# Performance work log

Hardware: AMD Instinct MI355X
Metric: run time of the kernel (lower is better)

## Reference

```python
import jax, jax.numpy as jnp
import numpy as np

L, B, E = 8192, 2, 1024
H, WS = 16, 256
D = E // H


def setup_inputs() -> dict:
    key = jax.random.key(0)
    ks = jax.random.split(key, 8)
    mk = lambda k: jax.random.normal(k, (E, E), dtype=jnp.float32) * 0.02
    return {
        'query': jax.random.normal(ks[0], (L, B, E), dtype=jnp.float32),
        'key':   jax.random.normal(ks[1], (L, B, E), dtype=jnp.float32),
        'value': jax.random.normal(ks[2], (L, B, E), dtype=jnp.float32),
        'Wq': mk(ks[3]), 'bq': jnp.zeros((E,), jnp.float32),
        'Wk': mk(ks[4]), 'bk': jnp.zeros((E,), jnp.float32),
        'Wv': mk(ks[5]), 'bv': jnp.zeros((E,), jnp.float32),
        'Wo': mk(ks[6]), 'bo': jnp.zeros((E,), jnp.float32),
    }


def reference(query, key, value, Wq, bq, Wk, bk, Wv, bv, Wo, bo):
    # Faithful translation, including the original's (B,L,H,D) layout and the
    # raw-memory view(B,H,L//ws,ws,D) reinterpretation of that layout.
    proj = lambda x, W, b: x @ W.T + b
    # (L,B,E) -> (L,B,H,D) -> transpose(0,1) -> (B,L,H,D)
    q = jnp.swapaxes(proj(query, Wq, bq).reshape(L, B, H, D), 0, 1)
    k = jnp.swapaxes(proj(key,   Wk, bk).reshape(L, B, H, D), 0, 1)
    v = jnp.swapaxes(proj(value, Wv, bv).reshape(L, B, H, D), 0, 1)
    # L > ws, L % ws == 0 -> pad_len = 0; contiguous().view == reshape
    nW = L // WS
    q = q.reshape(B, H, nW, WS, D)
    k = k.reshape(B, H, nW, WS, D)
    v = v.reshape(B, H, nW, WS, D)
    attn = jnp.einsum('bhnqd,bhnkd->bhnqk', q, k) / (D ** 0.5)
    attn = jax.nn.softmax(attn, axis=-1)
    out = jnp.einsum('bhnqk,bhnkd->bhnqd', attn, v)  # (B,H,nW,ws,D)
    out = out.reshape(B, H, L, D)
    # transpose(0,1).contiguous().view(L,B,E): reinterpret (H,B,L,D) memory
    out = jnp.swapaxes(out, 0, 1).reshape(L, B, E)
    return out @ Wo.T + bo
```

## Files before the change

kernel.cpp:

```cpp
#include <hip/hip_runtime.h>


typedef _Float16 half8 __attribute__((ext_vector_type(8)));
typedef _Float16 half4 __attribute__((ext_vector_type(4)));
typedef float    f32x4 __attribute__((ext_vector_type(4)));

#define MFMA16(a, b, c) __builtin_amdgcn_mfma_f32_16x16x32_f16((a), (b), (c), 0, 0, 0)
#define VM(n) asm volatile("s_waitcnt vmcnt(" #n ")" ::: "memory")
#define SCHED0 __builtin_amdgcn_sched_barrier(0)
#define LGKM0 do { asm volatile("s_waitcnt lgkmcnt(0)" ::: "memory"); SCHED0; } while (0)
#define BARW do { __builtin_amdgcn_s_barrier(); SCHED0; } while (0)

__device__ inline void gload16(const _Float16* g, _Float16* l) {
  __builtin_amdgcn_global_load_lds(
      (const __attribute__((address_space(1))) void*)g,
      (__attribute__((address_space(3))) void*)l, 16, 0, 0);
}

__device__ inline half8 cvt8(float4 a, float4 b) {
  half8 h = {(_Float16)a.x, (_Float16)a.y, (_Float16)a.z, (_Float16)a.w,
             (_Float16)b.x, (_Float16)b.y, (_Float16)b.z, (_Float16)b.w};
  return h;
}

__global__ __launch_bounds__(256) void cvt_fp16_k(const float* __restrict__ src,
                                                  _Float16* __restrict__ dst, int n) {
  int i = (blockIdx.x * 256 + threadIdx.x) * 8;
  if (i >= n) return;
  float4 a = *(const float4*)(src + i);
  float4 b = *(const float4*)(src + i + 4);
  *(half8*)(dst + i) = cvt8(a, b);
}

__global__ __launch_bounds__(256) void cvtw_k(const float* __restrict__ s0,
                                              const float* __restrict__ s1,
                                              const float* __restrict__ s2,
                                              const float* __restrict__ s3,
                                              _Float16* __restrict__ d) {
  const float* s = blockIdx.y == 0 ? s0 : blockIdx.y == 1 ? s1 : blockIdx.y == 2 ? s2 : s3;
  _Float16* dst = d + (size_t)blockIdx.y * (1 << 20);
  int i = (blockIdx.x * 256 + threadIdx.x) * 8;
  float4 a = *(const float4*)(s + i);
  float4 b = *(const float4*)(s + i + 4);
  *(half8*)(dst + i) = cvt8(a, b);
}

template <int OUT_F32>
__global__ __launch_bounds__(512) void gemm8p_k(const _Float16* __restrict__ Ah,
                                                const _Float16* __restrict__ Bw,
                                                const float* __restrict__ bias,
                                                void* __restrict__ Cout) {
  constexpr int K = 1024, NN = 1024, NT = 16;
  __shared__ alignas(16) _Float16 SH[65536];
  const int tid = threadIdx.x, lane = tid & 63, wave = tid >> 6;
  const int r15 = lane & 15, g = lane >> 4;
  const int wr = wave >> 2, wc = wave & 3;
  const int m0 = blockIdx.x * 256, n0 = blockIdx.y * 256;

  const int sp = tid >> 3;
  const int sv = (tid & 7) ^ (sp & 7);
  const int srow = 2 * sp + (sv >> 2);
  const int scol = (sv & 3) * 8;
  const int sdst = tid * 8;

  const int rp = r15 >> 1, rsub = r15 & 1;
  const int rslot = ((rsub * 4 + g) ^ rp) * 8;

  f32x4 acc[8][4] = {};
  half8 af[4], bf[4];

#define A_REGION(buf, kh) (&SH[(buf)*16384 + (kh)*8192])
#define B_REGION(buf, kh) (&SH[32768 + (buf)*16384 + (kh)*8192])

#define STAGE_B(t, buf, kh)                                                    \
  do {                                                                         \
    const _Float16* _s = Bw + (size_t)(n0 + srow) * K + (t)*64 + (kh)*32 + scol; \
    gload16(_s, B_REGION(buf, kh) + sdst);                                     \
    gload16(_s + (size_t)128 * K, B_REGION(buf, kh) + sdst + 4096);            \
  } while (0)

#define STAGE_A16(t, buf, kh)                                                  \
  do {                                                                         \
    const _Float16* _s = Ah + (size_t)(m0 + srow) * K + (t)*64 + (kh)*32 + scol; \
    gload16(_s, A_REGION(buf, kh) + sdst);                                     \
    gload16(_s + (size_t)128 * K, A_REGION(buf, kh) + sdst + 4096);            \
  } while (0)

#define READ_AF(buf, kk, MH)                                                   \
  do {                                                                         \
    _Float16* _b = A_REGION(buf, kk);                                          \
    int _pb = (wr * 64 + (MH)*32 + rp) * 64 + rslot;                           \
    af[0] = *(half8*)&_b[_pb];                                                 \
    af[1] = *(half8*)&_b[_pb + 512];                                           \
    af[2] = *(half8*)&_b[_pb + 1024];                                          \
    af[3] = *(half8*)&_b[_pb + 1536];                                          \
  } while (0)

#define READ_BF(buf, kk)                                                       \
  do {                                                                         \
    _Float16* _b = B_REGION(buf, kk);                                          \
    int _pb = (wc * 32 + rp) * 64 + rslot;                                     \
    bf[0] = *(half8*)&_b[_pb];                                                 \
    bf[1] = *(half8*)&_b[_pb + 512];                                           \
    bf[2] = *(half8*)&_b[_pb + 1024];                                          \
    bf[3] = *(half8*)&_b[_pb + 1536];                                          \
  } while (0)

#define MFMA_Q(MH)                                                             \
  do {                                                                         \
    __builtin_amdgcn_s_setprio(1);                                             \
    _Pragma("unroll") for (int mi = 0; mi < 4; mi++)                           \
        _Pragma("unroll") for (int ni = 0; ni < 4; ni++) acc[(MH)*4 + mi][ni] = \
        MFMA16(af[mi], bf[ni], acc[(MH)*4 + mi][ni]);                          \
    __builtin_amdgcn_s_setprio(0);                                             \
  } while (0)

  STAGE_A16(0, 0, 0);
  STAGE_A16(0, 0, 1);
  STAGE_B(0, 0, 0);
  STAGE_B(0, 0, 1);

  for (int t = 0; t < NT - 1; t++) {
    const int buf = t & 1, nb = buf ^ 1;
    STAGE_A16(t + 1, nb, 0);
    VM(4);
    SCHED0; BARW;
    READ_AF(buf, 0, 0);
    READ_BF(buf, 0);
    LGKM0;
    MFMA_Q(0);
    STAGE_A16(t + 1, nb, 1);
    READ_AF(buf, 0, 1);
    LGKM0;
    MFMA_Q(1);
    STAGE_B(t + 1, nb, 0);
    VM(6);
    SCHED0; BARW;
    READ_AF(buf, 1, 0);
    READ_BF(buf, 1);
    LGKM0;
    MFMA_Q(0);
    STAGE_B(t + 1, nb, 1);
    READ_AF(buf, 1, 1);
    LGKM0;
    MFMA_Q(1);
  }
  {
    VM(2);
    SCHED0; BARW;
    READ_AF(1, 0, 0);
    READ_BF(1, 0);
    LGKM0;
    MFMA_Q(0);
    READ_AF(1, 0, 1);
    LGKM0;
    MFMA_Q(1);
    VM(0);
    SCHED0; BARW;
    READ_AF(1, 1, 0);
    READ_BF(1, 1);
    LGKM0;
    MFMA_Q(0);
    READ_AF(1, 1, 1);
    LGKM0;
    MFMA_Q(1);
  }

#pragma unroll
  for (int ni = 0; ni < 4; ni++) {
    const int col = n0 + wc * 64 + ni * 16 + r15;
    const float bv = bias[col];
#pragma unroll
    for (int mi8 = 0; mi8 < 8; mi8++) {
      const int rowb = m0 + wr * 128 + mi8 * 16 + g * 4;
#pragma unroll
      for (int r = 0; r < 4; r++) {
        float x = acc[mi8][ni][r] + bv;
        if (OUT_F32)
          ((float*)Cout)[(size_t)(rowb + r) * NN + col] = x;
        else
          ((_Float16*)Cout)[(size_t)(rowb + r) * NN + col] = (_Float16)x;
      }
    }
  }
#undef A_REGION
#undef B_REGION
#undef STAGE_B
#undef STAGE_A16
#undef READ_AF
#undef READ_BF
#undef MFMA_Q
}

__global__ __launch_bounds__(256) void vtrans_k(const _Float16* __restrict__ Vp,
                                                _Float16* __restrict__ Vt) {
  const int c = blockIdx.x, b = blockIdx.y;
  __shared__ alignas(16) _Float16 Vl[256 * 64];
  const int tid = threadIdx.x;
  const int l0 = c * 16;
#pragma unroll
  for (int i = 0; i < 8; i++) {
    int q = tid + i * 256;
    int w = q >> 3, ck = q & 7;
    int ls = l0 + (w >> 4), h = w & 15;
    half8 v = *(const half8*)(Vp + (size_t)(ls * 2 + b) * 1024 + h * 64 + ck * 8);
    *(half8*)&Vl[w * 64 + (ck ^ (w & 7)) * 8] = v;
  }
  __syncthreads();
  const int d = tid >> 2, kcq = tid & 3;
  const size_t obase = ((size_t)(b * 512 + c) * 64 + d) * 256 + kcq * 64;
#pragma unroll
  for (int i8 = 0; i8 < 8; i8++) {
    half8 v;
#pragma unroll
    for (int j = 0; j < 8; j++) {
      int k = kcq * 64 + i8 * 8 + j;
      v[j] = Vl[k * 64 + (((d >> 3) ^ (k & 7)) * 8) + (d & 7)];
    }
    *(half8*)(Vt + obase + i8 * 8) = v;
  }
}

__global__ __launch_bounds__(512) void attn_win_k(const _Float16* __restrict__ Qp,
                                                  const _Float16* __restrict__ Kp,
                                                  const _Float16* __restrict__ Vt,
                                                  _Float16* __restrict__ Y) {
  const int c = blockIdx.x, b = blockIdx.y;
  __shared__ alignas(16) _Float16 Kl[256 * 64];
  __shared__ alignas(16) _Float16 Vl[64 * 256];
  const int tid = threadIdx.x, lane = tid & 63, wave = tid >> 6;
  const int i15 = lane & 15, g = lane >> 4;
  const int l0 = c * 16;

#pragma unroll
  for (int i = 0; i < 4; i++) {
    int q = tid + i * 512;
    int w = q >> 3, ck = q & 7;
    int ls = l0 + (w >> 4), h = w & 15;
    half8 v = *(const half8*)(Kp + (size_t)(ls * 2 + b) * 1024 + h * 64 + ck * 8);
    *(half8*)&Kl[w * 64 + (ck ^ (w & 7)) * 8] = v;
  }
  const size_t vb0 = (size_t)(b * 512 + c) * 64 * 256;
#pragma unroll
  for (int i = 0; i < 4; i++) {
    int q = tid + i * 512;
    int d = q >> 5, ck = q & 31;
    half8 v = *(const half8*)(Vt + vb0 + (size_t)d * 256 + ck * 8);
    *(half8*)&Vl[d * 256 + (ck ^ ((d & 7) << 2)) * 8] = v;
  }
  half8 qf[2][2];
#pragma unroll
  for (int wf = 0; wf < 2; wf++)
#pragma unroll
    for (int dh = 0; dh < 2; dh++) {
      int ls = l0 + wave * 2 + wf;
      qf[wf][dh] =
          *(const half8*)(Qp + (size_t)(ls * 2 + b) * 1024 + i15 * 64 + dh * 32 + g * 8);
    }
  __syncthreads();

  f32x4 acc[16][2] = {};
#pragma unroll
  for (int m = 0; m < 16; m++) {
    int row = m * 16 + i15;
    half8 a0 = *(half8*)&Kl[row * 64 + ((g) ^ (i15 & 7)) * 8];
    half8 a1 = *(half8*)&Kl[row * 64 + ((4 + g) ^ (i15 & 7)) * 8];
    acc[m][0] = MFMA16(a0, qf[0][0], acc[m][0]);
    acc[m][0] = MFMA16(a1, qf[0][1], acc[m][0]);
    acc[m][1] = MFMA16(a0, qf[1][0], acc[m][1]);
    acc[m][1] = MFMA16(a1, qf[1][1], acc[m][1]);
  }

#pragma unroll
  for (int wf = 0; wf < 2; wf++) {
    float mx = -3.0e38f;
#pragma unroll
    for (int m = 0; m < 16; m++)
#pragma unroll
      for (int r = 0; r < 4; r++) mx = fmaxf(mx, acc[m][wf][r]);
    mx = fmaxf(mx, __shfl_xor(mx, 16, 64));
    mx = fmaxf(mx, __shfl_xor(mx, 32, 64));
    float sum = 0.f;
#pragma unroll
    for (int m = 0; m < 16; m++)
#pragma unroll
      for (int r = 0; r < 4; r++) {
        float e = __expf((acc[m][wf][r] - mx) * 0.125f);
        acc[m][wf][r] = e;
        sum += e;
      }
    sum += __shfl_xor(sum, 16, 64);
    sum += __shfl_xor(sum, 32, 64);
    float inv = 1.f / sum;
#pragma unroll
    for (int m = 0; m < 16; m++)
#pragma unroll
      for (int r = 0; r < 4; r++) acc[m][wf][r] *= inv;
  }
  __syncthreads();

  _Float16* Pw = &Kl[wave * 2048];
  f32x4 oacc[2][4] = {};
#pragma unroll
  for (int kq = 0; kq < 4; kq++) {
#pragma unroll
    for (int wf = 0; wf < 2; wf++) {
      int rrow = wf * 16 + i15;
#pragma unroll
      for (int ml = 0; ml < 4; ml++) {
        f32x4 pv = acc[kq * 4 + ml][wf];
        half4 h = {(_Float16)pv[0], (_Float16)pv[1], (_Float16)pv[2], (_Float16)pv[3]};
        int ck = ml * 2 + (g >> 1);
        *(half4*)&Pw[rrow * 64 + ((ck ^ (i15 & 7)) * 8) + (g & 1) * 4] = h;
      }
    }
    asm volatile("s_waitcnt lgkmcnt(0)" ::: "memory");
    __builtin_amdgcn_sched_barrier(0);
#pragma unroll
    for (int kfl = 0; kfl < 2; kfl++) {
      half8 pa0 = *(half8*)&Pw[(i15)*64 + (((kfl * 4 + g) ^ (i15 & 7)) * 8)];
      half8 pa1 = *(half8*)&Pw[(16 + i15) * 64 + (((kfl * 4 + g) ^ (i15 & 7)) * 8)];
#pragma unroll
      for (int df = 0; df < 4; df++) {
        int drow = df * 16 + i15;
        half8 vbf =
            *(half8*)&Vl[drow * 256 + (((kq * 8 + kfl * 4 + g) ^ ((i15 & 7) << 2)) * 8)];
        oacc[0][df] = MFMA16(pa0, vbf, oacc[0][df]);
        oacc[1][df] = MFMA16(pa1, vbf, oacc[1][df]);
      }
    }
  }

  const int h2 = c >> 5, n = c & 31;
  const size_t yb = ((size_t)(h2 * 2 + b) * 8192 + (size_t)n * 256) * 64;
#pragma unroll
  for (int wf = 0; wf < 2; wf++)
#pragma unroll
    for (int df = 0; df < 4; df++)
#pragma unroll
      for (int r = 0; r < 4; r++) {
        int w = wave * 32 + wf * 16 + g * 4 + r;
        Y[yb + (size_t)w * 64 + df * 16 + i15] = (_Float16)oacc[wf][df][r];
      }
}

extern "C" void kernel_launch(void* const* d_in, const int* in_sizes, int n_in,
                              void* d_out, int out_size, void* d_ws, size_t ws_size,
                              hipStream_t stream) {
  const float* query = (const float*)d_in[0];
  const float* key_ = (const float*)d_in[1];
  const float* value = (const float*)d_in[2];
  const float* Wq = (const float*)d_in[3];
  const float* bq = (const float*)d_in[4];
  const float* Wk = (const float*)d_in[5];
  const float* bk = (const float*)d_in[6];
  const float* Wv = (const float*)d_in[7];
  const float* bv = (const float*)d_in[8];
  const float* Wo = (const float*)d_in[9];
  const float* bo = (const float*)d_in[10];

  _Float16* ws = (_Float16*)d_ws;
  _Float16* W16 = ws;
  _Float16* W16q = W16;
  _Float16* W16k = W16 + (1 << 20);
  _Float16* W16v = W16 + 2 * (1 << 20);
  _Float16* W16o = W16 + 3 * (1 << 20);
  _Float16* X16 = ws + 4 * (1 << 20);
  _Float16* Vp = X16 + (1 << 24);
  _Float16* Vt = X16;
  _Float16* Ybuf = Vp;

  _Float16* Qp = (_Float16*)d_out;
  _Float16* Kp = Qp + (1 << 24);

  cvtw_k<<<dim3(512, 4), 256, 0, stream>>>(Wq, Wk, Wv, Wo, W16);

  dim3 gg(64, 4), gb(512);

  cvt_fp16_k<<<8192, 256, 0, stream>>>(query, X16, 1 << 24);
  gemm8p_k<0><<<gg, gb, 0, stream>>>(X16, W16q, bq, (void*)Qp);

  cvt_fp16_k<<<8192, 256, 0, stream>>>(key_, X16, 1 << 24);
  gemm8p_k<0><<<gg, gb, 0, stream>>>(X16, W16k, bk, (void*)Kp);

  cvt_fp16_k<<<8192, 256, 0, stream>>>(value, X16, 1 << 24);
  gemm8p_k<0><<<gg, gb, 0, stream>>>(X16, W16v, bv, (void*)Vp);

  vtrans_k<<<dim3(512, 2), 256, 0, stream>>>(Vp, Vt);
  attn_win_k<<<dim3(512, 2), 512, 0, stream>>>(Qp, Kp, Vt, Ybuf);

  gemm8p_k<1><<<gg, gb, 0, stream>>>(Ybuf, W16o, bo, d_out);

  (void)in_sizes; (void)n_in; (void)out_size; (void)ws_size;
}
```

Measured before the change: 272.1 us.

## Fold softmax scale into Q projection, defer normalization, use exp2 and setprio

Folds the 1/sqrt(D) scale and the log2(e) factor into the Q projection epilogue, so the softmax can use a raw exp2 with no per-element multiply. Defers the 1/sum normalization to the output store, using shuffles to redistribute the per-row inverse, which removes a full pass of multiplies over the score tile. Also turns the max reduction into a tree and sets wave priority around the MFMA blocks. The cost is an extra multiply in every GEMM epilogue, and Q is rounded to fp16 after scaling, which changes numerics slightly.

Result: no change. 274.1 us (+0.7%).

```diff
diff --git a/kernel.cpp b/kernel.cpp
--- a/kernel.cpp
+++ b/kernel.cpp
@@ -49,7 +49,7 @@
 __global__ __launch_bounds__(512) void gemm8p_k(const _Float16* __restrict__ Ah,
                                                 const _Float16* __restrict__ Bw,
                                                 const float* __restrict__ bias,
-                                                void* __restrict__ Cout) {
+                                                void* __restrict__ Cout, float scale) {
   constexpr int K = 1024, NN = 1024, NT = 16;
   __shared__ alignas(16) _Float16 SH[65536];
   const int tid = threadIdx.x, lane = tid & 63, wave = tid >> 6;
@@ -175,7 +175,7 @@
       const int rowb = m0 + wr * 128 + mi8 * 16 + g * 4;
 #pragma unroll
       for (int r = 0; r < 4; r++) {
-        float x = acc[mi8][ni][r] + bv;
+        float x = (acc[mi8][ni][r] + bv) * scale;
         if (OUT_F32)
           ((float*)Cout)[(size_t)(rowb + r) * NN + col] = x;
         else
@@ -265,38 +265,57 @@
     int row = m * 16 + i15;
     half8 a0 = *(half8*)&Kl[row * 64 + ((g) ^ (i15 & 7)) * 8];
     half8 a1 = *(half8*)&Kl[row * 64 + ((4 + g) ^ (i15 & 7)) * 8];
+    __builtin_amdgcn_s_setprio(1);
     acc[m][0] = MFMA16(a0, qf[0][0], acc[m][0]);
     acc[m][0] = MFMA16(a1, qf[0][1], acc[m][0]);
     acc[m][1] = MFMA16(a0, qf[1][0], acc[m][1]);
     acc[m][1] = MFMA16(a1, qf[1][1], acc[m][1]);
-  }
-
+    __builtin_amdgcn_s_setprio(0);
+  }
+
+  float inv[2];
 #pragma unroll
   for (int wf = 0; wf < 2; wf++) {
-    float mx = -3.0e38f;
-#pragma unroll
-    for (int m = 0; m < 16; m++)
-#pragma unroll
-      for (int r = 0; r < 4; r++) mx = fmaxf(mx, acc[m][wf][r]);
+    f32x4 t[8];
+#pragma unroll
+    for (int i = 0; i < 8; i++) {
+#pragma unroll
+      for (int c4 = 0; c4 < 4; c4++)
+        t[i][c4] = fmaxf(acc[i][wf][c4], acc[i + 8][wf][c4]);
+    }
+#pragma unroll
+    for (int i = 0; i < 4; i++)
+#pragma unroll
+      for (int c4 = 0; c4 < 4; c4++) t[i][c4] = fmaxf(t[i][c4], t[i + 4][c4]);
+#pragma unroll
+    for (int i = 0; i < 2; i++)
+#pragma unroll
+      for (int c4 = 0; c4 < 4; c4++) t[i][c4] = fmaxf(t[i][c4], t[i + 2][c4]);
+#pragma unroll
+    for (int c4 = 0; c4 < 4; c4++) t[0][c4] = fmaxf(t[0][c4], t[1][c4]);
+    float mx = fmaxf(fmaxf(t[0][0], t[0][1]), fmaxf(t[0][2], t[0][3]));
     mx = fmaxf(mx, __shfl_xor(mx, 16, 64));
     mx = fmaxf(mx, __shfl_xor(mx, 32, 64));
-    float sum = 0.f;
-#pragma unroll
-    for (int m = 0; m < 16; m++)
-#pragma unroll
-      for (int r = 0; r < 4; r++) {
-        float e = __expf((acc[m][wf][r] - mx) * 0.125f);
-        acc[m][wf][r] = e;
-        sum += e;
+    f32x4 s4 = {0.f, 0.f, 0.f, 0.f};
+#pragma unroll
+    for (int m = 0; m < 16; m++) {
+#pragma unroll
+      for (int c4 = 0; c4 < 4; c4++) {
+        float e = __builtin_amdgcn_exp2f(acc[m][wf][c4] - mx);
+        acc[m][wf][c4] = e;
+        s4[c4] += e;
       }
+    }
+    float sum = (s4[0] + s4[1]) + (s4[2] + s4[3]);
     sum += __shfl_xor(sum, 16, 64);
     sum += __shfl_xor(sum, 32, 64);
-    float inv = 1.f / sum;
-#pragma unroll
-    for (int m = 0; m < 16; m++)
-#pragma unroll
-      for (int r = 0; r < 4; r++) acc[m][wf][r] *= inv;
-  }
+    inv[wf] = 1.f / sum;
+  }
+  float invv[2][4];
+#pragma unroll
+  for (int wf = 0; wf < 2; wf++)
+#pragma unroll
+    for (int r = 0; r < 4; r++) invv[wf][r] = __shfl(inv[wf], g * 4 + r, 64);
   __syncthreads();
 
   _Float16* Pw = &Kl[wave * 2048];
@@ -320,6 +339,7 @@
     for (int kfl = 0; kfl < 2; kfl++) {
       half8 pa0 = *(half8*)&Pw[(i15)*64 + (((kfl * 4 + g) ^ (i15 & 7)) * 8)];
       half8 pa1 = *(half8*)&Pw[(16 + i15) * 64 + (((kfl * 4 + g) ^ (i15 & 7)) * 8)];
+      __builtin_amdgcn_s_setprio(1);
 #pragma unroll
       for (int df = 0; df < 4; df++) {
         int drow = df * 16 + i15;
@@ -328,6 +348,7 @@
         oacc[0][df] = MFMA16(pa0, vbf, oacc[0][df]);
         oacc[1][df] = MFMA16(pa1, vbf, oacc[1][df]);
       }
+      __builtin_amdgcn_s_setprio(0);
     }
   }
 
@@ -340,7 +361,8 @@
 #pragma unroll
       for (int r = 0; r < 4; r++) {
         int w = wave * 32 + wf * 16 + g * 4 + r;
-        Y[yb + (size_t)w * 64 + df * 16 + i15] = (_Float16)oacc[wf][df][r];
+        Y[yb + (size_t)w * 64 + df * 16 + i15] =
+            (_Float16)(oacc[wf][df][r] * invv[wf][r]);
       }
 }
 
@@ -373,23 +395,25 @@
   _Float16* Qp = (_Float16*)d_out;
   _Float16* Kp = Qp + (1 << 24);
 
+  const float qscale = 0.125f * 1.44269504f;
+
   cvtw_k<<<dim3(512, 4), 256, 0, stream>>>(Wq, Wk, Wv, Wo, W16);
 
   dim3 gg(64, 4), gb(512);
 
   cvt_fp16_k<<<8192, 256, 0, stream>>>(query, X16, 1 << 24);
-  gemm8p_k<0><<<gg, gb, 0, stream>>>(X16, W16q, bq, (void*)Qp);
+  gemm8p_k<0><<<gg, gb, 0, stream>>>(X16, W16q, bq, (void*)Qp, qscale);
 
   cvt_fp16_k<<<8192, 256, 0, stream>>>(key_, X16, 1 << 24);
-  gemm8p_k<0><<<gg, gb, 0, stream>>>(X16, W16k, bk, (void*)Kp);
+  gemm8p_k<0><<<gg, gb, 0, stream>>>(X16, W16k, bk, (void*)Kp, 1.0f);
 
   cvt_fp16_k<<<8192, 256, 0, stream>>>(value, X16, 1 << 24);
-  gemm8p_k<0><<<gg, gb, 0, stream>>>(X16, W16v, bv, (void*)Vp);
+  gemm8p_k<0><<<gg, gb, 0, stream>>>(X16, W16v, bv, (void*)Vp, 1.0f);
 
   vtrans_k<<<dim3(512, 2), 256, 0, stream>>>(Vp, Vt);
   attn_win_k<<<dim3(512, 2), 512, 0, stream>>>(Qp, Kp, Vt, Ybuf);
 
-  gemm8p_k<1><<<gg, gb, 0, stream>>>(Ybuf, W16o, bo, d_out);
+  gemm8p_k<1><<<gg, gb, 0, stream>>>(Ybuf, W16o, bo, d_out, 1.0f);
 
   (void)in_sizes; (void)n_in; (void)out_size; (void)ws_size;
 }
```
